# Kernel optimization log

Measured on AMD Instinct MI355X. Metric: run time of the kernel, lower is better.

## Reference

```python
import jax, jax.numpy as jnp
import numpy as np
import math

L, D, H, V, B, S, MR = 8, 768, 12, 32000, 2, 1024, 4
HD = D // H

def setup_inputs() -> dict:
    key = jax.random.key(0)
    ks = iter(jax.random.split(key, 64))
    def rn(shape, s=0.02):
        return jax.random.normal(next(ks), shape, jnp.float32) * s
    inp = {}
    inp['tokens'] = jax.random.randint(next(ks), (B, S), 0, V, jnp.int32)
    inp['tok_emb'] = rn((V, D))
    inp['pos_emb'] = rn((S, D))
    for n in ['Wq_row', 'Wk_row', 'Wv_row', 'Wq_col', 'Wo']:
        inp[n] = rn((L, D, D))
    for n in ['bq_row', 'bk_row', 'bv_row', 'bq_col', 'bo']:
        inp[n] = jnp.zeros((L, D), jnp.float32)
    inp['ln1_g'] = jnp.ones((L, D), jnp.float32); inp['ln1_b'] = jnp.zeros((L, D), jnp.float32)
    inp['ln2_g'] = jnp.ones((L, D), jnp.float32); inp['ln2_b'] = jnp.zeros((L, D), jnp.float32)
    inp['W1'] = rn((L, D, MR * D)); inp['b1'] = jnp.zeros((L, MR * D), jnp.float32)
    inp['W2'] = rn((L, MR * D, D)); inp['b2'] = jnp.zeros((L, D), jnp.float32)
    inp['Wk_sh'] = rn((D, D)); inp['bk_sh'] = jnp.zeros((D,), jnp.float32)
    inp['Wv_sh'] = rn((D, D)); inp['bv_sh'] = jnp.zeros((D,), jnp.float32)
    inp['lnf_g'] = jnp.ones((D,), jnp.float32); inp['lnf_b'] = jnp.zeros((D,), jnp.float32)
    inp['Whead'] = rn((D, V)); inp['bhead'] = jnp.zeros((V,), jnp.float32)
    return inp

def _ln(x, g, b, eps=1e-5):
    m = x.mean(-1, keepdims=True)
    v = ((x - m) ** 2).mean(-1, keepdims=True)
    return (x - m) * jax.lax.rsqrt(v + eps) * g + b

def _heads(x):
    b, s, _ = x.shape
    return x.reshape(b, s, H, HD).transpose(0, 2, 1, 3)  # [B,H,S,hd]

def _merge(x):
    b, h, s, hd = x.shape
    return x.transpose(0, 2, 1, 3).reshape(b, s, h * hd)

def _forward(tokens, tok_emb, pos_emb, Wq_row, bq_row, Wk_row, bk_row, Wv_row, bv_row,
             Wq_col, bq_col, Wo, bo, ln1_g, ln1_b, ln2_g, ln2_b, W1, b1, W2, b2,
             Wk_sh, bk_sh, Wv_sh, bv_sh, lnf_g, lnf_b, Whead, bhead):
    s_len = tokens.shape[1]
    inv = 1.0 / math.sqrt(HD)
    x = tok_emb[tokens] + pos_emb[:s_len]
    mask = jnp.triu(jnp.ones((s_len, s_len), bool), 1)
    past_k, past_v = [], []
    for i in range(L):
        h = _ln(x, ln1_g[i], ln1_b[i])
        q_row = _heads(h @ Wq_row[i] + bq_row[i])
        k_row = _heads(h @ Wk_row[i] + bk_row[i])
        v_row = _heads(h @ Wv_row[i] + bv_row[i])
        q_col = _heads(h @ Wq_col[i] + bq_col[i])
        k_col = _heads(h @ Wk_sh + bk_sh)   # shared KV projector (archived memory)
        v_col = _heads(h @ Wv_sh + bv_sh)
        ts = jnp.einsum('bhqd,bhkd->bhqk', q_row, k_row) * inv
        ts = jnp.where(mask, -jnp.inf, ts)
        if past_k:
            pk = jnp.stack(past_k, axis=3)  # [B,H,S,l,hd]
            pv = jnp.stack(past_v, axis=3)
            ms = jnp.einsum('bhsd,bhsld->bhsl', q_col, pk) * inv
            w = jax.nn.softmax(jnp.concatenate([ts, ms], axis=-1), axis=-1)
            tw, mw = w[..., :s_len], w[..., s_len:]
            ctx = (jnp.einsum('bhqk,bhkd->bhqd', tw, v_row)
                   + jnp.einsum('bhsl,bhsld->bhsd', mw, pv))
        else:
            ctx = jnp.einsum('bhqk,bhkd->bhqd', jax.nn.softmax(ts, axis=-1), v_row)
        x = x + (_merge(ctx) @ Wo[i] + bo[i])
        h2 = _ln(x, ln2_g[i], ln2_b[i])
        x = x + (jax.nn.gelu(h2 @ W1[i] + b1[i], approximate=False) @ W2[i] + b2[i])
        past_k.append(k_col)
        past_v.append(v_col)
    return _ln(x, lnf_g, lnf_b) @ Whead + bhead

def reference(tokens, tok_emb, pos_emb, Wq_row, bq_row, Wk_row, bk_row, Wv_row, bv_row,
              Wq_col, bq_col, Wo, bo, ln1_g, ln1_b, ln2_g, ln2_b, W1, b1, W2, b2,
              Wk_sh, bk_sh, Wv_sh, bv_sh, lnf_g, lnf_b, Whead, bhead):
    return _forward(tokens, tok_emb, pos_emb, Wq_row, bq_row, Wk_row, bk_row, Wv_row, bv_row,
                    Wq_col, bq_col, Wo, bo, ln1_g, ln1_b, ln2_g, ln2_b, W1, b1, W2, b2,
                    Wk_sh, bk_sh, Wv_sh, bv_sh, lnf_g, lnf_b, Whead, bhead)
```

## Files before the change

kernel.cpp:

```cpp
#include <hip/hip_runtime.h>
#include <hip/hip_bf16.h>
#include <math.h>

#define L_   8
#define D_   768
#define H_   12
#define V_   32000
#define B_   2
#define S_   1024
#define HD_  64
#define BS_  2048
#define DFF_ 3072

typedef __hip_bfloat16 bf16;
typedef __attribute__((ext_vector_type(8))) short bf16x8;
typedef __attribute__((ext_vector_type(4))) float f32x4;

#define CFUN(r) (((r) >> 1) & 3)

__device__ __forceinline__ void cp16(void* lds, const void* g) {
  __builtin_amdgcn_global_load_lds(
      (const __attribute__((address_space(1))) void*)g,
      (__attribute__((address_space(3))) void*)lds, 16, 0, 0);
}

__device__ __forceinline__ unsigned short f2bf(float v) {
  __hip_bfloat16 h = __float2bfloat16(v);
  return *reinterpret_cast<unsigned short*>(&h);
}
__device__ __forceinline__ float bf2f(unsigned short u) {
  return __uint_as_float(((unsigned)u) << 16);
}

__global__ __launch_bounds__(256) void k_embedln(const int* __restrict__ tokens,
    const float* __restrict__ tok_emb, const float* __restrict__ pos_emb,
    const float* __restrict__ g, const float* __restrict__ b,
    float* __restrict__ x, bf16* __restrict__ out) {
  const int row = blockIdx.x;
  const int t = threadIdx.x;
  const int s = row & (S_ - 1);
  const int tok = tokens[row];
  const size_t base = (size_t)row * D_;
  const float* te = tok_emb + (size_t)tok * D_;
  const float* pe = pos_emb + (size_t)s * D_;
  float v0 = te[t] + pe[t];
  float v1 = te[t + 256] + pe[t + 256];
  float v2 = te[t + 512] + pe[t + 512];
  x[base + t] = v0; x[base + t + 256] = v1; x[base + t + 512] = v2;
  float sum  = v0 + v1 + v2;
  float s2 = v0 * v0 + v1 * v1 + v2 * v2;
#pragma unroll
  for (int off = 32; off; off >>= 1) {
    sum += __shfl_down(sum, off);
    s2  += __shfl_down(s2, off);
  }
  __shared__ float rs[4], rs2[4];
  __shared__ float mean_s, rstd_s;
  int wid = t >> 6;
  if ((t & 63) == 0) { rs[wid] = sum; rs2[wid] = s2; }
  __syncthreads();
  if (t == 0) {
    float S1 = rs[0] + rs[1] + rs[2] + rs[3];
    float S2 = rs2[0] + rs2[1] + rs2[2] + rs2[3];
    float m  = S1 / D_;
    float var = S2 / D_ - m * m;
    mean_s = m;
    rstd_s = rsqrtf(var + 1e-5f);
  }
  __syncthreads();
  float m = mean_s, r = rstd_s;
  bf16* orow = out + base;
  orow[t]       = __float2bfloat16((v0 - m) * r * g[t]       + b[t]);
  orow[t + 256] = __float2bfloat16((v1 - m) * r * g[t + 256] + b[t + 256]);
  orow[t + 512] = __float2bfloat16((v2 - m) * r * g[t + 512] + b[t + 512]);
}

__global__ __launch_bounds__(192) void k_redln(float* __restrict__ x,
    const float* __restrict__ pk, const float* __restrict__ b2,
    const float* __restrict__ g, const float* __restrict__ b,
    bf16* __restrict__ out) {
  const int row = blockIdx.x;
  const int t = threadIdx.x;
  const int c = t * 4;
  const size_t base = (size_t)row * D_;
  const size_t MN = (size_t)BS_ * D_;
  float4 xv = *reinterpret_cast<const float4*>(x + base + c);
  float4 p0 = *reinterpret_cast<const float4*>(pk + base + c);
  float4 p1 = *reinterpret_cast<const float4*>(pk + MN + base + c);
  float4 bv = *reinterpret_cast<const float4*>(b2 + c);
  float4 v;
  v.x = xv.x + p0.x + p1.x + bv.x;
  v.y = xv.y + p0.y + p1.y + bv.y;
  v.z = xv.z + p0.z + p1.z + bv.z;
  v.w = xv.w + p0.w + p1.w + bv.w;
  *reinterpret_cast<float4*>(x + base + c) = v;
  float s  = v.x + v.y + v.z + v.w;
  float s2 = v.x * v.x + v.y * v.y + v.z * v.z + v.w * v.w;
#pragma unroll
  for (int off = 32; off; off >>= 1) {
    s  += __shfl_down(s, off);
    s2 += __shfl_down(s2, off);
  }
  __shared__ float rs[3], rs2[3];
  __shared__ float mean_s, rstd_s;
  const int wid = t >> 6;
  if ((t & 63) == 0) { rs[wid] = s; rs2[wid] = s2; }
  __syncthreads();
  if (t == 0) {
    float S1 = rs[0] + rs[1] + rs[2];
    float S2 = rs2[0] + rs2[1] + rs2[2];
    float m  = S1 / D_;
    float var = S2 / D_ - m * m;
    mean_s = m;
    rstd_s = rsqrtf(var + 1e-5f);
  }
  __syncthreads();
  const float m = mean_s, r = rstd_s;
  float4 gv = *reinterpret_cast<const float4*>(g + c);
  float4 bb = *reinterpret_cast<const float4*>(b + c);
  ushort4 o;
  o.x = f2bf((v.x - m) * r * gv.x + bb.x);
  o.y = f2bf((v.y - m) * r * gv.y + bb.y);
  o.z = f2bf((v.z - m) * r * gv.z + bb.z);
  o.w = f2bf((v.w - m) * r * gv.w + bb.w);
  *reinterpret_cast<ushort4*>((unsigned short*)out + base + c) = o;
}

__device__ __forceinline__ void conv_tile64(const float* __restrict__ Wsrc,
    int N, int K, bf16* __restrict__ Wdst, int n0, int k0,
    float (*t)[65], int tid) {
  const int ro = tid >> 4;
  const int cq = (tid & 15) * 4;
#pragma unroll
  for (int i = 0; i < 4; i++) {
    const int row = i * 16 + ro;
    float4 v = *reinterpret_cast<const float4*>(
        Wsrc + (size_t)(k0 + row) * N + n0 + cq);
    t[row][cq] = v.x; t[row][cq + 1] = v.y;
    t[row][cq + 2] = v.z; t[row][cq + 3] = v.w;
  }
  __syncthreads();
  const int ks = (tid & 7) * 8;
  const int nn0 = tid >> 3;
#pragma unroll
  for (int pass = 0; pass < 2; pass++) {
    const int n = nn0 + pass * 32;
    bf16x8 ov;
#pragma unroll
    for (int j = 0; j < 8; j++) ov[j] = (short)f2bf(t[ks + j][n]);
    *reinterpret_cast<bf16x8*>(
        (unsigned short*)Wdst + (size_t)(n0 + n) * K + k0 + ks) = ov;
  }
}

#define TILE_DD   144
#define C_WQ      1152
#define C_WK      2304
#define C_WQC     3456
#define C_WV      4608
#define C_WKSH    4752
#define C_WVSH    4896
#define C_WO      6048
#define C_W1      10656
#define C_W2      15264
#define C_WHEAD   21264
#define C_BIAS    21408
#define W6S_      ((size_t)3072 * 768)
#define DD_       ((size_t)768 * 768)
#define DF_       ((size_t)768 * 3072)

__global__ __launch_bounds__(256) void k_wconv(
    const float* __restrict__ Wq, const float* __restrict__ Wk,
    const float* __restrict__ Wqc, const float* __restrict__ Wv,
    const float* __restrict__ Wksh, const float* __restrict__ Wvsh,
    const float* __restrict__ Wo, const float* __restrict__ W1,
    const float* __restrict__ W2, const float* __restrict__ Whead,
    bf16* __restrict__ tW6, bf16* __restrict__ tWsh, bf16* __restrict__ tWo,
    bf16* __restrict__ tW1, bf16* __restrict__ tW2, bf16* __restrict__ tWhead,
    const float* __restrict__ bq, const float* __restrict__ bk,
    const float* __restrict__ bqc, const float* __restrict__ bv,
    const float* __restrict__ bksh, const float* __restrict__ bvsh,
    float* __restrict__ b6) {
  __shared__ float t[64][65];
  const int idx = blockIdx.x;
  const int tid = threadIdx.x;

  if (idx < C_WV) {
    int sect, tt;
    const float* src;
    if (idx < C_WQ)       { sect = 0; tt = idx;          src = Wq;  }
    else if (idx < C_WK)  { sect = 1; tt = idx - C_WQ;   src = Wk;  }
    else if (idx < C_WQC) { sect = 2; tt = idx - C_WK;   src = Wqc; }
    else                  { sect = 3; tt = idx - C_WQC;  src = Wv;  }
    const int z = tt / TILE_DD, rem = tt - z * TILE_DD;
    conv_tile64(src + (size_t)z * DD_, 768, 768,
                tW6 + (size_t)z * W6S_ + (size_t)sect * DD_,
                (rem % 12) * 64, (rem / 12) * 64, t, tid);
  } else if (idx < C_WVSH) {
    const float* src = (idx < C_WKSH) ? Wksh : Wvsh;
    bf16* dst = (idx < C_WKSH) ? tWsh : (tWsh + DD_);
    const int rem = (idx < C_WKSH) ? (idx - C_WV) : (idx - C_WKSH);
    conv_tile64(src, 768, 768, dst, (rem % 12) * 64, (rem / 12) * 64, t, tid);
  } else if (idx < C_WO) {
    const int tt = idx - C_WVSH;
    const int z = tt / TILE_DD, rem = tt - z * TILE_DD;
    conv_tile64(Wo + (size_t)z * DD_, 768, 768, tWo + (size_t)z * DD_,
                (rem % 12) * 64, (rem / 12) * 64, t, tid);
  } else if (idx < C_W1) {
    const int tt = idx - C_WO;
    const int z = tt / 576, rem = tt - z * 576;
    conv_tile64(W1 + (size_t)z * DF_, 3072, 768, tW1 + (size_t)z * DF_,
                (rem % 48) * 64, (rem / 48) * 64, t, tid);
  } else if (idx < C_W2) {
    const int tt = idx - C_W1;
    const int z = tt / 576, rem = tt - z * 576;
    conv_tile64(W2 + (size_t)z * DF_, 768, 3072, tW2 + (size_t)z * DF_,
                (rem % 12) * 64, (rem / 12) * 64, t, tid);
  } else if (idx < C_WHEAD) {
    const int tt = idx - C_W2;
    conv_tile64(Whead, 32000, 768, tWhead, (tt % 500) * 64, (tt / 500) * 64,
                t, tid);
  } else {
    const int i2 = (idx - C_WHEAD) * 256 + tid;
    if (i2 < L_ * 4608) {
      const int l = i2 / 4608, c = i2 - l * 4608;
      float v = (c < 768)  ? bq[l * 768 + c]
              : (c < 1536) ? bk[l * 768 + c - 768]
              : (c < 2304) ? bqc[l * 768 + c - 1536]
              : (c < 3072) ? bv[l * 768 + c - 2304]
              : (c < 3840) ? bksh[c - 3072]
                           : bvsh[c - 3840];
      b6[i2] = v;
    }
  }
}

template <int BM, int EPI, int KSPL>
__global__ __launch_bounds__(256) void k_bgemm(
    const bf16* __restrict__ A, const bf16* __restrict__ Wt,
    const float* __restrict__ bias, const float* __restrict__ resid,
    float* __restrict__ Cf, bf16* __restrict__ Cb,
    int NM, int M, int N, int K) {
  constexpr int ASZ = BM * 64;
  constexpr int ALINES = BM / 64;
  constexpr int BSTRIDE = ASZ + 8192;
  constexpr int MF = BM / 32;
  __shared__ __align__(16) char smem[3 * BSTRIDE];
  const int tid = threadIdx.x;
  const int l = tid & 63, w = tid >> 6;
  const int wr = w >> 1, wc = w & 1;

  const int nwg = (int)gridDim.x;
  int id = (int)blockIdx.x;
  id = (id & 7) * (nwg >> 3) + (id >> 3);
  int sk = 0;
  if constexpr (KSPL == 2) {
    const int TT = nwg >> 1;
    sk = id / TT;
    id -= sk * TT;
  }
  const int m0 = (id % NM) * BM;
  const int n0 = (id / NM) * 128;
  const int kstart = sk * (K / KSPL);

  const int lane15 = l & 15, lg = l >> 4;

  const int r0 = tid >> 2, p0 = tid & 3;
  const char* aSrc[ALINES];
#pragma unroll
  for (int i = 0; i < ALINES; i++) {
    const int rr = i * 64 + r0;
    aSrc[i] = (const char*)(A + (size_t)(m0 + rr) * K + kstart) + ((p0 ^ CFUN(rr)) * 16);
  }
  const char* bSrc0 = (const char*)(Wt + (size_t)(n0 + r0) * K + kstart) + ((p0 ^ CFUN(r0)) * 16);
  const char* bSrc1 = (const char*)(Wt + (size_t)(n0 + 64 + r0) * K + kstart) + ((p0 ^ CFUN(64 + r0)) * 16);

  int aOff[MF], bOff[4];
#pragma unroll
  for (int mi = 0; mi < MF; mi++) {
    int r = wr * (BM / 2) + mi * 16 + lane15;
    aOff[mi] = r * 64 + ((lg ^ CFUN(r)) * 16);
  }
#pragma unroll
  for (int ni = 0; ni < 4; ni++) {
    int r = wc * 64 + ni * 16 + lane15;
    bOff[ni] = ASZ + r * 64 + ((lg ^ CFUN(r)) * 16);
  }

  f32x4 acc[MF][4];
#pragma unroll
  for (int mi = 0; mi < MF; mi++)
#pragma unroll
    for (int ni = 0; ni < 4; ni++) acc[mi][ni] = (f32x4){0.f, 0.f, 0.f, 0.f};

  auto stage = [&](int buf, int t) {
    const size_t kb = (size_t)t * 64;
    char* base = smem + buf * BSTRIDE;
#pragma unroll
    for (int i = 0; i < ALINES; i++)
      cp16(base + i * 4096 + w * 1024, aSrc[i] + kb);
    cp16(base + ASZ + w * 1024, bSrc0 + kb);
    cp16(base + ASZ + 4096 + w * 1024, bSrc1 + kb);
  };
  auto compute = [&](int buf) {
    const char* base = smem + buf * BSTRIDE;
    bf16x8 af[MF], bfr[4];
#pragma unroll
    for (int mi = 0; mi < MF; mi++) af[mi] = *(const bf16x8*)(base + aOff[mi]);
#pragma unroll
    for (int ni = 0; ni < 4; ni++) bfr[ni] = *(const bf16x8*)(base + bOff[ni]);
    __builtin_amdgcn_s_setprio(1);
#pragma unroll
    for (int mi = 0; mi < MF; mi++)
#pragma unroll
      for (int ni = 0; ni < 4; ni++)
        acc[mi][ni] = __builtin_amdgcn_mfma_f32_16x16x32_bf16(
            af[mi], bfr[ni], acc[mi][ni], 0, 0, 0);
    __builtin_amdgcn_s_setprio(0);
  };

  const int nk = (K / KSPL) >> 5;
  stage(0, 0);
  stage(1, 1);
  int buf = 0;
  for (int t = 0; t < nk; t++) {
    if (t + 1 < nk) {
      if constexpr (ALINES == 2) asm volatile("s_waitcnt vmcnt(4)" ::: "memory");
      else                       asm volatile("s_waitcnt vmcnt(3)" ::: "memory");
    } else {
      asm volatile("s_waitcnt vmcnt(0)" ::: "memory");
    }
    __builtin_amdgcn_s_barrier();
    if (t + 2 < nk) {
      int nb = buf + 2; if (nb >= 3) nb -= 3;
      stage(nb, t + 2);
    }
    compute(buf);
    buf = (buf == 2) ? 0 : buf + 1;
  }

#pragma unroll
  for (int ni = 0; ni < 4; ni++) {
    const int col = n0 + wc * 64 + ni * 16 + lane15;
    const float bv = bias[col];
#pragma unroll
    for (int mi = 0; mi < MF; mi++) {
      const int rowb = m0 + wr * (BM / 2) + mi * 16 + lg * 4;
      if constexpr (EPI == 7) {
#pragma unroll
        for (int j = 0; j < 4; j++)
          Cf[(size_t)sk * M * N + (size_t)(rowb + j) * N + col] = acc[mi][ni][j];
      } else {
#pragma unroll
        for (int j = 0; j < 4; j++) {
          const int row = rowb + j;
          float v = acc[mi][ni][j] + bv;
          if constexpr (EPI == 1) v += resid[(size_t)row * N + col];
          if constexpr (EPI == 2) {
            v = 0.5f * v * (1.0f + erff(v * 0.70710678118654752f));
            Cb[(size_t)row * N + col] = __float2bfloat16(v);
          } else if constexpr (EPI == 3) {
            Cb[(size_t)row * N + col] = __float2bfloat16(v);
          } else {
            Cf[(size_t)row * N + col] = v;
          }
        }
      }
    }
  }
}

#define HBAR() asm volatile("s_barrier" ::: "memory")
#define MFMA16(AF, BF, MB, NB)                                               \
  do {                                                                       \
    __builtin_amdgcn_s_setprio(1);                                           \
    _Pragma("unroll") for (int mi_ = 0; mi_ < 4; mi_++)                      \
      _Pragma("unroll") for (int ni_ = 0; ni_ < 2; ni_++)                    \
        _Pragma("unroll") for (int ks_ = 0; ks_ < 2; ks_++)                  \
          acc[(MB) + mi_][(NB) + ni_] =                                      \
              __builtin_amdgcn_mfma_f32_16x16x32_bf16(                       \
                  AF[mi_][ks_], BF[ni_][ks_], acc[(MB) + mi_][(NB) + ni_],   \
                  0, 0, 0);                                                  \
    __builtin_amdgcn_s_setprio(0);                                           \
  } while (0)

template <int EPI>
__global__ __launch_bounds__(512, 1) void k_g8(const bf16* __restrict__ A,
    const bf16* __restrict__ Wt, const bf16* __restrict__ Wt2,
    const float* __restrict__ bias, float* __restrict__ Cf,
    bf16* __restrict__ Cb, bf16* __restrict__ Cb2, bf16* __restrict__ Cb3) {
  __shared__ __align__(16) char smem[131072];
  const int tid = threadIdx.x;
  const int l = tid & 63, w = tid >> 6;
  const int wr = w >> 2, wc = w & 3;
  const int lane15 = l & 15, lg = l >> 4;

  const int nwg = (int)gridDim.x;
  int id = (int)blockIdx.x;
  id = (id & 7) * (nwg >> 3) + (id >> 3);
  const int m0 = (id % 8) * 256;
  const int n0 = (id / 8) * 256;

  const bf16* WB = Wt;
  int nb0 = n0;
  if constexpr (EPI == 6) {
    if (n0 >= 3072) { WB = Wt2; nb0 = n0 - 3072; }
  }

  auto issueA = [&](int tile, int hb) {
#pragma unroll
    for (int j = 0; j < 2; j++) {
      const int idx = j * 512 + tid;
      const int rl = idx >> 3, sl = idx & 7;
      const bf16* g = A + (size_t)(m0 + hb + rl) * 768 + tile * 64 +
                      ((sl ^ (rl & 7)) << 3);
      cp16(smem + (tile & 1) * 32768 + hb * 128 + (j * 512 + w * 64) * 16, g);
    }
  };
  auto issueB = [&](int tile, int hb) {
#pragma unroll
    for (int j = 0; j < 2; j++) {
      const int idx = j * 512 + tid;
      const int rl = idx >> 3, sl = idx & 7;
      const bf16* g = WB + (size_t)(nb0 + hb + rl) * 768 + tile * 64 +
                      ((sl ^ (rl & 7)) << 3);
      cp16(smem + 65536 + (tile & 1) * 32768 + hb * 128 + (j * 512 + w * 64) * 16, g);
    }
  };
  auto ldA = [&](int buf, int mi, int ks) {
    const int r = wr * 128 + mi * 16 + lane15;
    return *(const bf16x8*)(smem + buf * 32768 + r * 128 +
                            ((((ks << 2) + lg) ^ (r & 7)) << 4));
  };
  auto ldB = [&](int buf, int ni, int ks) {
    const int r = wc * 64 + ni * 16 + lane15;
    return *(const bf16x8*)(smem + 65536 + buf * 32768 + r * 128 +
                            ((((ks << 2) + lg) ^ (r & 7)) << 4));
  };

  f32x4 acc[8][4];
#pragma unroll
  for (int i = 0; i < 8; i++)
#pragma unroll
    for (int j = 0; j < 4; j++) acc[i][j] = (f32x4){0.f, 0.f, 0.f, 0.f};
  bf16x8 alo[4][2], ahi[4][2], blo[2][2], bhi[2][2];

  issueA(0, 0);  issueA(0, 128);  issueB(0, 0);  issueB(0, 128);
  issueB(1, 0);  issueA(1, 0);    issueB(1, 128);
  asm volatile("s_waitcnt vmcnt(6)" ::: "memory");
  HBAR();

  for (int it = 0; it < 5; ++it) {
    const int Tb = 2 * it + 1, Tn = 2 * it + 2;
#pragma unroll
    for (int mi = 0; mi < 4; mi++) { alo[mi][0] = ldA(0, mi, 0); alo[mi][1] = ldA(0, mi, 1); }
#pragma unroll
    for (int ni = 0; ni < 2; ni++) { blo[ni][0] = ldB(0, ni, 0); blo[ni][1] = ldB(0, ni, 1); }
    issueA(Tb, 128);
    HBAR(); MFMA16(alo, blo, 0, 0); HBAR();
#pragma unroll
    for (int ni = 0; ni < 2; ni++) { bhi[ni][0] = ldB(0, ni + 2, 0); bhi[ni][1] = ldB(0, ni + 2, 1); }
    HBAR(); MFMA16(alo, bhi, 0, 2); HBAR();
#pragma unroll
    for (int mi = 0; mi < 4; mi++) { ahi[mi][0] = ldA(0, mi + 4, 0); ahi[mi][1] = ldA(0, mi + 4, 1); }
    issueB(Tn, 0);
    HBAR(); MFMA16(ahi, bhi, 4, 2); HBAR();
    issueA(Tn, 0);
    issueB(Tn, 128);
    asm volatile("s_waitcnt vmcnt(6)" ::: "memory");
    HBAR(); MFMA16(ahi, blo, 4, 0); HBAR();
#pragma unroll
    for (int mi = 0; mi < 4; mi++) { alo[mi][0] = ldA(1, mi, 0); alo[mi][1] = ldA(1, mi, 1); }
#pragma unroll
    for (int ni = 0; ni < 2; ni++) { blo[ni][0] = ldB(1, ni, 0); blo[ni][1] = ldB(1, ni, 1); }
    issueA(Tn, 128);
    HBAR(); MFMA16(alo, blo, 0, 0); HBAR();
#pragma unroll
    for (int ni = 0; ni < 2; ni++) { bhi[ni][0] = ldB(1, ni + 2, 0); bhi[ni][1] = ldB(1, ni + 2, 1); }
    HBAR(); MFMA16(alo, bhi, 0, 2); HBAR();
#pragma unroll
    for (int mi = 0; mi < 4; mi++) { ahi[mi][0] = ldA(1, mi + 4, 0); ahi[mi][1] = ldA(1, mi + 4, 1); }
    issueB(Tn + 1, 0);
    HBAR(); MFMA16(ahi, bhi, 4, 2); HBAR();
    issueA(Tn + 1, 0);
    issueB(Tn + 1, 128);
    asm volatile("s_waitcnt vmcnt(6)" ::: "memory");
    HBAR(); MFMA16(ahi, blo, 4, 0); HBAR();
  }

  {
#pragma unroll
    for (int mi = 0; mi < 4; mi++) { alo[mi][0] = ldA(0, mi, 0); alo[mi][1] = ldA(0, mi, 1); }
#pragma unroll
    for (int ni = 0; ni < 2; ni++) { blo[ni][0] = ldB(0, ni, 0); blo[ni][1] = ldB(0, ni, 1); }
    issueA(11, 128);
    HBAR(); MFMA16(alo, blo, 0, 0); HBAR();
#pragma unroll
    for (int ni = 0; ni < 2; ni++) { bhi[ni][0] = ldB(0, ni + 2, 0); bhi[ni][1] = ldB(0, ni + 2, 1); }
    HBAR(); MFMA16(alo, bhi, 0, 2); HBAR();
#pragma unroll
    for (int mi = 0; mi < 4; mi++) { ahi[mi][0] = ldA(0, mi + 4, 0); ahi[mi][1] = ldA(0, mi + 4, 1); }
    HBAR(); MFMA16(ahi, bhi, 4, 2); HBAR();
    asm volatile("s_waitcnt vmcnt(0)" ::: "memory");
    HBAR(); MFMA16(ahi, blo, 4, 0); HBAR();
#pragma unroll
    for (int mi = 0; mi < 4; mi++) { alo[mi][0] = ldA(1, mi, 0); alo[mi][1] = ldA(1, mi, 1); }
#pragma unroll
    for (int ni = 0; ni < 2; ni++) { blo[ni][0] = ldB(1, ni, 0); blo[ni][1] = ldB(1, ni, 1); }
    MFMA16(alo, blo, 0, 0);
#pragma unroll
    for (int ni = 0; ni < 2; ni++) { bhi[ni][0] = ldB(1, ni + 2, 0); bhi[ni][1] = ldB(1, ni + 2, 1); }
    MFMA16(alo, bhi, 0, 2);
#pragma unroll
    for (int mi = 0; mi < 4; mi++) { ahi[mi][0] = ldA(1, mi + 4, 0); ahi[mi][1] = ldA(1, mi + 4, 1); }
    MFMA16(ahi, bhi, 4, 2);
    MFMA16(ahi, blo, 4, 0);
  }

#pragma unroll
  for (int ni = 0; ni < 4; ni++) {
    const int col = n0 + wc * 64 + ni * 16 + lane15;
    const float bv = bias[col];
#pragma unroll
    for (int mi = 0; mi < 8; mi++) {
      const int rowb = m0 + wr * 128 + mi * 16 + lg * 4;
      if constexpr (EPI == 0) {
#pragma unroll
        for (int j = 0; j < 4; j++)
          Cf[(size_t)(rowb + j) * 32000 + col] = acc[mi][ni][j] + bv;
      } else {
        if (col < 2304) {
#pragma unroll
          for (int j = 0; j < 4; j++)
            Cb[(size_t)(rowb + j) * 2304 + col] = __float2bfloat16(acc[mi][ni][j] + bv);
        } else if (col < 3072) {
          ushort4 pk;
          pk.x = f2bf(acc[mi][ni][0] + bv);
          pk.y = f2bf(acc[mi][ni][1] + bv);
          pk.z = f2bf(acc[mi][ni][2] + bv);
          pk.w = f2bf(acc[mi][ni][3] + bv);
          const int bq = rowb >> 10, s = rowb & (S_ - 1);
          *reinterpret_cast<ushort4*>(
              (unsigned short*)Cb2 + ((size_t)(bq * 768 + (col - 2304))) * S_ + s) = pk;
        } else {
#pragma unroll
          for (int j = 0; j < 4; j++)
            Cb3[(size_t)(rowb + j) * 1536 + (col - 3072)] =
                __float2bfloat16(acc[mi][ni][j] + bv);
        }
      }
    }
  }
}

__global__ __launch_bounds__(256) void k_attn(
    const bf16* __restrict__ qkv, const bf16* __restrict__ vT,
    const bf16* __restrict__ memkv, bf16* __restrict__ ctx, int layer) {
  const int bh = blockIdx.x;
  const int b = bh / H_, h = bh % H_;
  const int qt = (int)gridDim.y - 1 - (int)blockIdx.y;
  const int tid = threadIdx.x;
  const int w = tid >> 6, l = tid & 63;
  const int lane15 = l & 15, lg = l >> 4;
  const float inv = 0.125f;

  __shared__ char plds[4][2048];
  __shared__ float wlp[4][16][16];
  char* pl = plds[w];

  const int qrow0 = qt * 64 + w * 16;
  const size_t rowA = (size_t)(b * S_ + qrow0 + lane15);
  const bf16* qp = qkv + rowA * 2304 + h * 64 + lg * 8;
  auto scale8 = [](bf16x8 v) {
    bf16x8 r;
#pragma unroll
    for (int e = 0; e < 8; e++)
      r[e] = (short)f2bf(bf2f((unsigned short)v[e]) * 0.125f);
    return r;
  };
  const bf16x8 qf0 = scale8(*(const bf16x8*)(qp));
  const bf16x8 qf1 = scale8(*(const bf16x8*)(qp + 32));

  const bf16* kbase = qkv + (size_t)(b * S_) * 2304 + 768 + h * 64 + lg * 8;
  const bf16* vbase = vT + ((size_t)(b * 768 + h * 64 + lane15)) * S_;

  float mrow[4], dsum[4];
  f32x4 acc[4];
#pragma unroll
  for (int j = 0; j < 4; j++) { mrow[j] = -INFINITY; dsum[j] = 0.f; }
#pragma unroll
  for (int ni = 0; ni < 4; ni++) acc[ni] = (f32x4){0.f, 0.f, 0.f, 0.f};

  const int ntile = ((qrow0 + 15) >> 6) + 1;
  for (int kt64 = 0; kt64 < ntile; kt64++) {
    const int k0 = kt64 * 64;
    f32x4 sc[4];
#pragma unroll
    for (int kt = 0; kt < 4; kt++) {
      const bf16* kp = kbase + (size_t)(k0 + kt * 16 + lane15) * 2304;
      bf16x8 kf0 = *(const bf16x8*)(kp);
      bf16x8 kf1 = *(const bf16x8*)(kp + 32);
      f32x4 z = (f32x4){0.f, 0.f, 0.f, 0.f};
      z = __builtin_amdgcn_mfma_f32_16x16x32_bf16(qf0, kf0, z, 0, 0, 0);
      sc[kt] = __builtin_amdgcn_mfma_f32_16x16x32_bf16(qf1, kf1, z, 0, 0, 0);
    }
    float tmax[4];
#pragma unroll
    for (int j = 0; j < 4; j++) tmax[j] = -INFINITY;
    const bool needMask = (k0 + 63 > qrow0);
    if (needMask) {
#pragma unroll
      for (int kt = 0; kt < 4; kt++) {
        const int kabs = k0 + kt * 16 + lane15;
#pragma unroll
        for (int j = 0; j < 4; j++) {
          const int qabs = qrow0 + lg * 4 + j;
          float v = (kabs <= qabs) ? sc[kt][j] : -INFINITY;
          sc[kt][j] = v;
          tmax[j] = fmaxf(tmax[j], v);
        }
      }
    } else {
#pragma unroll
      for (int kt = 0; kt < 4; kt++)
#pragma unroll
        for (int j = 0; j < 4; j++) tmax[j] = fmaxf(tmax[j], sc[kt][j]);
    }
#pragma unroll
    for (int off = 1; off < 16; off <<= 1)
#pragma unroll
      for (int j = 0; j < 4; j++) tmax[j] = fmaxf(tmax[j], __shfl_xor(tmax[j], off, 16));

    bool grow = false;
#pragma unroll
    for (int j = 0; j < 4; j++) grow |= (tmax[j] > mrow[j]);
    if (__ballot(grow) != 0ull) {
#pragma unroll
      for (int j = 0; j < 4; j++) {
        const float mnew = fmaxf(mrow[j], tmax[j]);
        const float alpha = __expf(mrow[j] - mnew);
        mrow[j] = mnew;
        dsum[j] *= alpha;
#pragma unroll
        for (int ni = 0; ni < 4; ni++) acc[ni][j] *= alpha;
      }
    }
    float psum[4] = {0.f, 0.f, 0.f, 0.f};
#pragma unroll
    for (int kt = 0; kt < 4; kt++) {
      const int gsl = kt * 2 + (lane15 >> 3);
      const int ebyte = (lane15 & 7) * 2;
#pragma unroll
      for (int j = 0; j < 4; j++) {
        const float p = __expf(sc[kt][j] - mrow[j]);
        psum[j] += p;
        const int r = lg * 4 + j;
        *(unsigned short*)(pl + r * 128 + ((gsl ^ (r & 7)) << 4) + ebyte) = f2bf(p);
      }
    }
#pragma unroll
    for (int off = 1; off < 16; off <<= 1)
#pragma unroll
      for (int j = 0; j < 4; j++) psum[j] += __shfl_xor(psum[j], off, 16);
#pragma unroll
    for (int j = 0; j < 4; j++) dsum[j] += psum[j];

#pragma unroll
    for (int ks = 0; ks < 2; ks++) {
      bf16x8 pa = *(const bf16x8*)(pl + lane15 * 128 +
                                   ((((ks << 2) + lg) ^ (lane15 & 7)) << 4));
      const bf16* vp = vbase + k0 + ks * 32 + lg * 8;
#pragma unroll
      for (int ni = 0; ni < 4; ni++) {
        bf16x8 vf = *(const bf16x8*)(vp + (size_t)ni * 16 * S_);
        acc[ni] = __builtin_amdgcn_mfma_f32_16x16x32_bf16(pa, vf, acc[ni], 0, 0, 0);
      }
    }
  }

  const int r4 = lg * 4;
  if (lane15 < layer) {
    const int ml = lane15;
#pragma unroll
    for (int j = 0; j < 4; j++) {
      const size_t rowB = (size_t)(b * S_) + qrow0 + r4 + j;
      const bf16* qc = qkv + rowB * 2304 + 1536 + h * 64;
      const bf16* mk = memkv + ((size_t)ml * BS_ + rowB) * 1536 + h * 64;
      float d_ = 0.f;
#pragma unroll
      for (int t = 0; t < 8; t++) {
        bf16x8 qv = *(const bf16x8*)(qc + t * 8);
        bf16x8 kv = *(const bf16x8*)(mk + t * 8);
#pragma unroll
        for (int e = 0; e < 8; e++)
          d_ += bf2f((unsigned short)qv[e]) * bf2f((unsigned short)kv[e]);
      }
      wlp[w][r4 + j][ml] = d_ * inv;
    }
  }
  if (layer > 0) {
#pragma unroll
    for (int j = 0; j < 4; j++) {
      const int r = r4 + j;
      float mm = -INFINITY;
      for (int ml = 0; ml < layer; ml++) mm = fmaxf(mm, wlp[w][r][ml]);
      const float mnew = fmaxf(mrow[j], mm);
      const float alpha = __expf(mrow[j] - mnew);
      mrow[j] = mnew;
      dsum[j] *= alpha;
#pragma unroll
      for (int ni = 0; ni < 4; ni++) acc[ni][j] *= alpha;
      const size_t rowB = (size_t)(b * S_) + qrow0 + r;
      for (int ml = 0; ml < layer; ml++) {
        const float p = __expf(wlp[w][r][ml] - mnew);
        dsum[j] += p;
        const unsigned short* mv = (const unsigned short*)(memkv +
            ((size_t)ml * BS_ + rowB) * 1536 + 768 + h * 64 + lane15);
#pragma unroll
        for (int ni = 0; ni < 4; ni++)
          acc[ni][j] += p * bf2f(mv[ni * 16]);
      }
    }
  }

#pragma unroll
  for (int j = 0; j < 4; j++) {
    const float rd = 1.f / dsum[j];
    const size_t rowB = (size_t)(b * S_) + qrow0 + r4 + j;
    bf16* cp = ctx + rowB * 768 + h * 64 + lane15;
#pragma unroll
    for (int ni = 0; ni < 4; ni++)
      cp[ni * 16] = __float2bfloat16(acc[ni][j] * rd);
  }
}

extern "C" void kernel_launch(void* const* d_in, const int* in_sizes, int n_in,
                              void* d_out, int out_size, void* d_ws, size_t ws_size,
                              hipStream_t stream) {
  const int*   tokens  = (const int*)d_in[0];
  const float* tok_emb = (const float*)d_in[1];
  const float* pos_emb = (const float*)d_in[2];
  const float *Wq_row, *Wk_row, *Wv_row, *Wq_col, *Wo;
  const float *bq_row, *bk_row, *bv_row, *bq_col, *bo;
  if (in_sizes[4] == L_ * D_ * D_) {
    Wq_row = (const float*)d_in[3];  Wk_row = (const float*)d_in[4];
    Wv_row = (const float*)d_in[5];  Wq_col = (const float*)d_in[6];
    Wo     = (const float*)d_in[7];
    bq_row = (const float*)d_in[8];  bk_row = (const float*)d_in[9];
    bv_row = (const float*)d_in[10]; bq_col = (const float*)d_in[11];
    bo     = (const float*)d_in[12];
  } else {
    Wq_row = (const float*)d_in[3];  bq_row = (const float*)d_in[4];
    Wk_row = (const float*)d_in[5];  bk_row = (const float*)d_in[6];
    Wv_row = (const float*)d_in[7];  bv_row = (const float*)d_in[8];
    Wq_col = (const float*)d_in[9];  bq_col = (const float*)d_in[10];
    Wo     = (const float*)d_in[11]; bo     = (const float*)d_in[12];
  }
  const float* ln1_g = (const float*)d_in[13]; const float* ln1_b = (const float*)d_in[14];
  const float* ln2_g = (const float*)d_in[15]; const float* ln2_b = (const float*)d_in[16];
  const float* W1    = (const float*)d_in[17]; const float* b1    = (const float*)d_in[18];
  const float* W2    = (const float*)d_in[19]; const float* b2    = (const float*)d_in[20];
  const float* Wk_sh = (const float*)d_in[21]; const float* bk_sh = (const float*)d_in[22];
  const float* Wv_sh = (const float*)d_in[23]; const float* bv_sh = (const float*)d_in[24];
  const float* lnf_g = (const float*)d_in[25]; const float* lnf_b = (const float*)d_in[26];
  const float* Whead = (const float*)d_in[27]; const float* bhead = (const float*)d_in[28];

  char* p = (char*)d_ws;
  float* x      = (float*)p; p += (size_t)BS_ * D_ * 4;
  bf16*  h_bf   = (bf16*)p;  p += (size_t)BS_ * D_ * 2;
  bf16*  qkv3   = (bf16*)p;  p += (size_t)BS_ * 2304 * 2;
  bf16*  vTb    = (bf16*)p;  p += (size_t)B_ * 768 * S_ * 2;
  bf16*  memkv  = (bf16*)p;  p += (size_t)L_ * BS_ * 1536 * 2;
  bf16*  ctx_bf = (bf16*)p;  p += (size_t)BS_ * D_ * 2;
  bf16*  mlp_bf = (bf16*)p;  p += (size_t)BS_ * DFF_ * 2;
  float* pkbuf  = (float*)p; p += (size_t)2 * BS_ * D_ * 4;
  float* b6cat  = (float*)p; p += (size_t)L_ * 4608 * 4;
  bf16* tW6    = (bf16*)p; p += (size_t)L_ * 3072 * D_ * 2;
  bf16* tWsh   = (bf16*)p; p += (size_t)1536 * D_ * 2;
  bf16* tWo    = (bf16*)p; p += (size_t)L_ * D_ * D_ * 2;
  bf16* tW1    = (bf16*)p; p += (size_t)L_ * DFF_ * D_ * 2;
  bf16* tW2    = (bf16*)p; p += (size_t)L_ * D_ * DFF_ * 2;
  bf16* tWhead = (bf16*)p; p += (size_t)V_ * D_ * 2;

  k_wconv<<<dim3(C_BIAS), 256, 0, stream>>>(
      Wq_row, Wk_row, Wq_col, Wv_row, Wk_sh, Wv_sh, Wo, W1, W2, Whead,
      tW6, tWsh, tWo, tW1, tW2, tWhead,
      bq_row, bk_row, bq_col, bv_row, bk_sh, bv_sh, b6cat);

  k_embedln<<<dim3(BS_), 256, 0, stream>>>(tokens, tok_emb, pos_emb,
                                           ln1_g, ln1_b, x, h_bf);

  const size_t DD = (size_t)D_ * D_;
  const size_t W6S = (size_t)3072 * 768;
  for (int i = 0; i < L_; i++) {
    k_g8<6><<<dim3(144), 512, 0, stream>>>(
        h_bf, tW6 + (size_t)i * W6S, tWsh, b6cat + (size_t)i * 4608,
        nullptr, qkv3, vTb, memkv + (size_t)i * BS_ * 1536);
    k_attn<<<dim3(B_ * H_, S_ / 64), 256, 0, stream>>>(qkv3, vTb, memkv, ctx_bf, i);
    k_bgemm<64, 7, 2><<<dim3(384), 256, 0, stream>>>(
        ctx_bf, tWo + (size_t)i * DD, bo + i * D_,
        nullptr, pkbuf, nullptr, 32, BS_, 768, 768);
    k_redln<<<dim3(BS_), 192, 0, stream>>>(x, pkbuf, bo + i * D_,
                                           ln2_g + i * D_, ln2_b + i * D_, h_bf);
    k_bgemm<128, 2, 1><<<dim3(384), 256, 0, stream>>>(
        h_bf, tW1 + (size_t)i * 3072 * 768, b1 + (size_t)i * DFF_,
        nullptr, nullptr, mlp_bf, 16, BS_, 3072, 768);
    k_bgemm<64, 7, 2><<<dim3(384), 256, 0, stream>>>(
        mlp_bf, tW2 + (size_t)i * 768 * 3072, b2 + i * D_,
        nullptr, pkbuf, nullptr, 32, BS_, 768, 3072);
    const float* gn = (i < L_ - 1) ? (ln1_g + (i + 1) * D_) : lnf_g;
    const float* bn = (i < L_ - 1) ? (ln1_b + (i + 1) * D_) : lnf_b;
    k_redln<<<dim3(BS_), 192, 0, stream>>>(x, pkbuf, b2 + i * D_, gn, bn, h_bf);
  }
  k_g8<0><<<dim3(1000), 512, 0, stream>>>(h_bf, tWhead, nullptr, bhead,
                                          (float*)d_out, nullptr, nullptr, nullptr);
}
```

Measured before the change: 1.560 ms.

## Use 4-way split-K with 128-row tiles for W2 GEMM; widen weight-convert tiles

The W2 down-projection GEMM switches from 64-row tiles with 2-way split-K to 128-row tiles with 4-way split-K. Its partial-sum buffer doubles, and the following reduce+LayerNorm kernel is templated to sum a variable number of partial slabs. Separately, the weight transpose/convert kernel now processes 64x256 tiles per block instead of 64x64, cutting block count and giving wider coalesced reads. The costs are more partial-sum traffic in the reduction and larger LDS use per conversion block.

```diff
diff --git a/kernel.cpp b/kernel.cpp
--- a/kernel.cpp
+++ b/kernel.cpp
@@ -75,6 +75,7 @@
   orow[t + 512] = __float2bfloat16((v2 - m) * r * g[t + 512] + b[t + 512]);
 }
 
+template <int NPK>
 __global__ __launch_bounds__(192) void k_redln(float* __restrict__ x,
     const float* __restrict__ pk, const float* __restrict__ b2,
     const float* __restrict__ g, const float* __restrict__ b,
@@ -84,15 +85,14 @@
   const int c = t * 4;
   const size_t base = (size_t)row * D_;
   const size_t MN = (size_t)BS_ * D_;
-  float4 xv = *reinterpret_cast<const float4*>(x + base + c);
-  float4 p0 = *reinterpret_cast<const float4*>(pk + base + c);
-  float4 p1 = *reinterpret_cast<const float4*>(pk + MN + base + c);
+  float4 v = *reinterpret_cast<const float4*>(x + base + c);
   float4 bv = *reinterpret_cast<const float4*>(b2 + c);
-  float4 v;
-  v.x = xv.x + p0.x + p1.x + bv.x;
-  v.y = xv.y + p0.y + p1.y + bv.y;
-  v.z = xv.z + p0.z + p1.z + bv.z;
-  v.w = xv.w + p0.w + p1.w + bv.w;
+  v.x += bv.x; v.y += bv.y; v.z += bv.z; v.w += bv.w;
+#pragma unroll
+  for (int sslab = 0; sslab < NPK; sslab++) {
+    float4 pv = *reinterpret_cast<const float4*>(pk + (size_t)sslab * MN + base + c);
+    v.x += pv.x; v.y += pv.y; v.z += pv.z; v.w += pv.w;
+  }
   *reinterpret_cast<float4*>(x + base + c) = v;
   float s  = v.x + v.y + v.z + v.w;
   float s2 = v.x * v.x + v.y * v.y + v.z * v.z + v.w * v.w;
@@ -126,24 +126,25 @@
   *reinterpret_cast<ushort4*>((unsigned short*)out + base + c) = o;
 }
 
-__device__ __forceinline__ void conv_tile64(const float* __restrict__ Wsrc,
+__device__ __forceinline__ void conv_tile256(const float* __restrict__ Wsrc,
     int N, int K, bf16* __restrict__ Wdst, int n0, int k0,
-    float (*t)[65], int tid) {
-  const int ro = tid >> 4;
-  const int cq = (tid & 15) * 4;
-#pragma unroll
-  for (int i = 0; i < 4; i++) {
-    const int row = i * 16 + ro;
+    float (*t)[261], int tid) {
+  const int lane = tid & 63, wv = tid >> 6;
+#pragma unroll
+  for (int it = 0; it < 16; it++) {
+    const int row = wv * 16 + it;
     float4 v = *reinterpret_cast<const float4*>(
-        Wsrc + (size_t)(k0 + row) * N + n0 + cq);
-    t[row][cq] = v.x; t[row][cq + 1] = v.y;
-    t[row][cq + 2] = v.z; t[row][cq + 3] = v.w;
+        Wsrc + (size_t)(k0 + row) * N + n0 + lane * 4);
+    t[row][lane * 4]     = v.x;
+    t[row][lane * 4 + 1] = v.y;
+    t[row][lane * 4 + 2] = v.z;
+    t[row][lane * 4 + 3] = v.w;
   }
   __syncthreads();
   const int ks = (tid & 7) * 8;
   const int nn0 = tid >> 3;
 #pragma unroll
-  for (int pass = 0; pass < 2; pass++) {
+  for (int pass = 0; pass < 8; pass++) {
     const int n = nn0 + pass * 32;
     bf16x8 ov;
 #pragma unroll
@@ -153,18 +154,18 @@
   }
 }
 
-#define TILE_DD   144
-#define C_WQ      1152
-#define C_WK      2304
-#define C_WQC     3456
-#define C_WV      4608
-#define C_WKSH    4752
-#define C_WVSH    4896
-#define C_WO      6048
-#define C_W1      10656
-#define C_W2      15264
-#define C_WHEAD   21264
-#define C_BIAS    21408
+#define TILE_DD   36
+#define C_WQ      288
+#define C_WK      576
+#define C_WQC     864
+#define C_WV      1152
+#define C_WKSH    1188
+#define C_WVSH    1224
+#define C_WO      1512
+#define C_W1      2664
+#define C_W2      3816
+#define C_WHEAD   5316
+#define C_BIAS    5460
 #define W6S_      ((size_t)3072 * 768)
 #define DD_       ((size_t)768 * 768)
 #define DF_       ((size_t)768 * 3072)
@@ -181,7 +182,7 @@
     const float* __restrict__ bqc, const float* __restrict__ bv,
     const float* __restrict__ bksh, const float* __restrict__ bvsh,
     float* __restrict__ b6) {
-  __shared__ float t[64][65];
+  __shared__ float t[64][261];
   const int idx = blockIdx.x;
   const int tid = threadIdx.x;
 
@@ -193,33 +194,35 @@
     else if (idx < C_WQC) { sect = 2; tt = idx - C_WK;   src = Wqc; }
     else                  { sect = 3; tt = idx - C_WQC;  src = Wv;  }
     const int z = tt / TILE_DD, rem = tt - z * TILE_DD;
-    conv_tile64(src + (size_t)z * DD_, 768, 768,
-                tW6 + (size_t)z * W6S_ + (size_t)sect * DD_,
-                (rem % 12) * 64, (rem / 12) * 64, t, tid);
+    conv_tile256(src + (size_t)z * DD_, 768, 768,
+                 tW6 + (size_t)z * W6S_ + (size_t)sect * DD_,
+                 (rem % 3) * 256, (rem / 3) * 64, t, tid);
+  } else if (idx < C_WKSH) {
+    const int rem = idx - C_WV;
+    conv_tile256(Wksh, 768, 768, tWsh, (rem % 3) * 256, (rem / 3) * 64, t, tid);
   } else if (idx < C_WVSH) {
-    const float* src = (idx < C_WKSH) ? Wksh : Wvsh;
-    bf16* dst = (idx < C_WKSH) ? tWsh : (tWsh + DD_);
-    const int rem = (idx < C_WKSH) ? (idx - C_WV) : (idx - C_WKSH);
-    conv_tile64(src, 768, 768, dst, (rem % 12) * 64, (rem / 12) * 64, t, tid);
+    const int rem = idx - C_WKSH;
+    conv_tile256(Wvsh, 768, 768, tWsh + DD_, (rem % 3) * 256, (rem / 3) * 64,
+                 t, tid);
   } else if (idx < C_WO) {
     const int tt = idx - C_WVSH;
     const int z = tt / TILE_DD, rem = tt - z * TILE_DD;
-    conv_tile64(Wo + (size_t)z * DD_, 768, 768, tWo + (size_t)z * DD_,
-                (rem % 12) * 64, (rem / 12) * 64, t, tid);
+    conv_tile256(Wo + (size_t)z * DD_, 768, 768, tWo + (size_t)z * DD_,
+                 (rem % 3) * 256, (rem / 3) * 64, t, tid);
   } else if (idx < C_W1) {
     const int tt = idx - C_WO;
-    const int z = tt / 576, rem = tt - z * 576;
-    conv_tile64(W1 + (size_t)z * DF_, 3072, 768, tW1 + (size_t)z * DF_,
-                (rem % 48) * 64, (rem / 48) * 64, t, tid);
+    const int z = tt / 144, rem = tt - z * 144;
+    conv_tile256(W1 + (size_t)z * DF_, 3072, 768, tW1 + (size_t)z * DF_,
+                 (rem % 12) * 256, (rem / 12) * 64, t, tid);
   } else if (idx < C_W2) {
     const int tt = idx - C_W1;
-    const int z = tt / 576, rem = tt - z * 576;
-    conv_tile64(W2 + (size_t)z * DF_, 768, 3072, tW2 + (size_t)z * DF_,
-                (rem % 12) * 64, (rem / 12) * 64, t, tid);
+    const int z = tt / 144, rem = tt - z * 144;
+    conv_tile256(W2 + (size_t)z * DF_, 768, 3072, tW2 + (size_t)z * DF_,
+                 (rem % 3) * 256, (rem / 3) * 64, t, tid);
   } else if (idx < C_WHEAD) {
     const int tt = idx - C_W2;
-    conv_tile64(Whead, 32000, 768, tWhead, (tt % 500) * 64, (tt / 500) * 64,
-                t, tid);
+    conv_tile256(Whead, 32000, 768, tWhead, (tt % 125) * 256, (tt / 125) * 64,
+                 t, tid);
   } else {
     const int i2 = (idx - C_WHEAD) * 256 + tid;
     if (i2 < L_ * 4608) {
@@ -254,8 +257,8 @@
   int id = (int)blockIdx.x;
   id = (id & 7) * (nwg >> 3) + (id >> 3);
   int sk = 0;
-  if constexpr (KSPL == 2) {
-    const int TT = nwg >> 1;
+  if constexpr (KSPL > 1) {
+    const int TT = nwg / KSPL;
     sk = id / TT;
     id -= sk * TT;
   }
@@ -773,7 +776,7 @@
   bf16*  memkv  = (bf16*)p;  p += (size_t)L_ * BS_ * 1536 * 2;
   bf16*  ctx_bf = (bf16*)p;  p += (size_t)BS_ * D_ * 2;
   bf16*  mlp_bf = (bf16*)p;  p += (size_t)BS_ * DFF_ * 2;
-  float* pkbuf  = (float*)p; p += (size_t)2 * BS_ * D_ * 4;
+  float* pkbuf  = (float*)p; p += (size_t)4 * BS_ * D_ * 4;
   float* b6cat  = (float*)p; p += (size_t)L_ * 4608 * 4;
   bf16* tW6    = (bf16*)p; p += (size_t)L_ * 3072 * D_ * 2;
   bf16* tWsh   = (bf16*)p; p += (size_t)1536 * D_ * 2;
@@ -800,17 +803,17 @@
     k_bgemm<64, 7, 2><<<dim3(384), 256, 0, stream>>>(
         ctx_bf, tWo + (size_t)i * DD, bo + i * D_,
         nullptr, pkbuf, nullptr, 32, BS_, 768, 768);
-    k_redln<<<dim3(BS_), 192, 0, stream>>>(x, pkbuf, bo + i * D_,
-                                           ln2_g + i * D_, ln2_b + i * D_, h_bf);
+    k_redln<2><<<dim3(BS_), 192, 0, stream>>>(x, pkbuf, bo + i * D_,
+                                              ln2_g + i * D_, ln2_b + i * D_, h_bf);
     k_bgemm<128, 2, 1><<<dim3(384), 256, 0, stream>>>(
         h_bf, tW1 + (size_t)i * 3072 * 768, b1 + (size_t)i * DFF_,
         nullptr, nullptr, mlp_bf, 16, BS_, 3072, 768);
-    k_bgemm<64, 7, 2><<<dim3(384), 256, 0, stream>>>(
+    k_bgemm<128, 7, 4><<<dim3(384), 256, 0, stream>>>(
         mlp_bf, tW2 + (size_t)i * 768 * 3072, b2 + i * D_,
-        nullptr, pkbuf, nullptr, 32, BS_, 768, 3072);
+        nullptr, pkbuf, nullptr, 16, BS_, 768, 3072);
     const float* gn = (i < L_ - 1) ? (ln1_g + (i + 1) * D_) : lnf_g;
     const float* bn = (i < L_ - 1) ? (ln1_b + (i + 1) * D_) : lnf_b;
-    k_redln<<<dim3(BS_), 192, 0, stream>>>(x, pkbuf, b2 + i * D_, gn, bn, h_bf);
+    k_redln<4><<<dim3(BS_), 192, 0, stream>>>(x, pkbuf, b2 + i * D_, gn, bn, h_bf);
   }
   k_g8<0><<<dim3(1000), 512, 0, stream>>>(h_bf, tWhead, nullptr, bhead,
                                           (float*)d_out, nullptr, nullptr, nullptr);
```

Result: no change. 1.569 ms (+0.6%).
